# Performance work log

Hardware: AMD Instinct MI355X
Metric: run time of the kernel (lower is better)

Reference implementation:

```python
import jax, jax.numpy as jnp
import numpy as np

D_MODEL = 2048
N_HEADS = 32
N_KV_HEADS = 8
HEAD_DIM = D_MODEL // N_HEADS  # 64
THETA = 10000.0
BATCH = 2
SEQ = 2048


def _rope_tables(seq_len, head_dim, theta):
    idx = jnp.arange(0, head_dim, 2, dtype=jnp.float32)
    inv_freq = 1.0 / (theta ** (idx / head_dim))
    pos = jnp.arange(seq_len, dtype=jnp.float32)
    angles = pos[:, None] * inv_freq[None, :]  # (S, head_dim/2)
    return jnp.cos(angles), jnp.sin(angles)


def _apply_rope(x, cos, sin):
    # x: (B, H, S, Dh); cos/sin: (S, Dh/2)
    c = cos[None, None, :, :]
    s = sin[None, None, :, :]
    x_even = x[..., 0::2]
    x_odd = x[..., 1::2]
    out_even = x_even * c - x_odd * s
    out_odd = x_even * s + x_odd * c
    # interleave back: stack on last axis and reshape
    return jnp.stack([out_even, out_odd], axis=-1).reshape(x.shape)


def setup_inputs() -> dict:
    key = jax.random.key(0)
    kx, kq, kk, kv, ko = jax.random.split(key, 5)
    std_sq = (2.0 / (D_MODEL + D_MODEL)) ** 0.5
    std_kv = (2.0 / (D_MODEL + N_KV_HEADS * HEAD_DIM)) ** 0.5
    return {
        "x": jax.random.normal(kx, (BATCH, SEQ, D_MODEL), dtype=jnp.float32),
        "Wq": jax.random.normal(kq, (D_MODEL, D_MODEL), dtype=jnp.float32) * std_sq,
        "Wk": jax.random.normal(kk, (N_KV_HEADS * HEAD_DIM, D_MODEL), dtype=jnp.float32) * std_kv,
        "Wv": jax.random.normal(kv, (N_KV_HEADS * HEAD_DIM, D_MODEL), dtype=jnp.float32) * std_kv,
        "Wo": jax.random.normal(ko, (D_MODEL, D_MODEL), dtype=jnp.float32) * std_sq,
    }


def reference(x, Wq, Wk, Wv, Wo):
    B, S, D = x.shape
    groups = N_HEADS // N_KV_HEADS
    cos, sin = _rope_tables(S, HEAD_DIM, THETA)

    q = (x @ Wq.T).reshape(B, S, N_HEADS, HEAD_DIM).transpose(0, 2, 1, 3)
    k = (x @ Wk.T).reshape(B, S, N_KV_HEADS, HEAD_DIM).transpose(0, 2, 1, 3)
    v = (x @ Wv.T).reshape(B, S, N_KV_HEADS, HEAD_DIM).transpose(0, 2, 1, 3)

    q = _apply_rope(q, cos, sin)
    k = _apply_rope(k, cos, sin)

    # GQA: repeat kv heads (repeat_interleave along head dim)
    k = jnp.repeat(k, groups, axis=1)  # (B, H, S, Dh)
    v = jnp.repeat(v, groups, axis=1)

    scale = 1.0 / jnp.sqrt(jnp.float32(HEAD_DIM))
    scores = jnp.einsum('bhqd,bhkd->bhqk', q, k) * scale
    causal = jnp.tril(jnp.ones((S, S), dtype=bool))
    scores = jnp.where(causal[None, None, :, :], scores, -jnp.inf)
    attn = jax.nn.softmax(scores, axis=-1)
    out = jnp.einsum('bhqk,bhkd->bhqd', attn, v)
    out = out.transpose(0, 2, 1, 3).reshape(B, S, D)
    return out @ Wo.T
```

## Files before the change

### kernel.cpp

```cpp
#include <hip/hip_runtime.h>
#include <math.h>

#define BATCHN 2
#define SEQ 2048
#define DMODEL 2048
#define NH 32
#define NKV 8
#define HDIM 64
#define KVD 512
#define ROWS 4096

typedef __bf16 bf16x8 __attribute__((ext_vector_type(8)));
typedef float f32x4 __attribute__((ext_vector_type(4)));
typedef unsigned short u16x8 __attribute__((ext_vector_type(8)));

#define MFMA(a, b, c) __builtin_amdgcn_mfma_f32_16x16x32_bf16(a, b, c, 0, 0, 0)

__device__ __forceinline__ unsigned short f2bf(float f) {
  union { float f; unsigned u; } v; v.f = f;
  unsigned u = v.u;
  u += 0x7fffu + ((u >> 16) & 1u);
  return (unsigned short)(u >> 16);
}

__device__ __forceinline__ unsigned cvtpk(float a, float b) {
  unsigned r;
  asm("v_cvt_pk_bf16_f32 %0, %1, %2" : "=v"(r) : "v"(a), "v"(b));
  return r;
}
__device__ __forceinline__ void pl32(unsigned& a, unsigned& b) {
  asm("v_permlane32_swap_b32 %0, %1" : "+v"(a), "+v"(b));
}
__device__ __forceinline__ void pl16(unsigned& a, unsigned& b) {
  asm("v_permlane16_swap_b32 %0, %1" : "+v"(a), "+v"(b));
}
__device__ __forceinline__ float exp2v(float x) {
  float r;
  asm("v_exp_f32 %0, %1" : "=v"(r) : "v"(x));
  return r;
}

__device__ __forceinline__ void gload16(const void* g, void* l) {
  __builtin_amdgcn_global_load_lds((const __attribute__((address_space(1))) unsigned int*)g,
                                   (__attribute__((address_space(3))) unsigned int*)l, 16, 0, 0);
}

#define FENCE() asm volatile("" ::: "memory")
#define BARRIER() do { FENCE(); __builtin_amdgcn_s_barrier(); FENCE(); } while (0)
#define VMCNT(n) asm volatile("s_waitcnt vmcnt(" #n ")" ::: "memory")

__global__ __launch_bounds__(256) void conv_all(const float* __restrict__ x,
                                                const float* __restrict__ Wq,
                                                const float* __restrict__ Wk,
                                                const float* __restrict__ Wv,
                                                const float* __restrict__ Wo,
                                                unsigned short* __restrict__ xb,
                                                unsigned short* __restrict__ Wqb,
                                                unsigned short* __restrict__ Wkb,
                                                unsigned short* __restrict__ Wvb,
                                                unsigned short* __restrict__ Wob,
                                                float* __restrict__ ct,
                                                float* __restrict__ st) {
  int i = blockIdx.x * 256 + threadIdx.x;
  const float* in;
  unsigned short* out;
  int off;
  if (i < 2097152)      { in = x;  out = xb;  off = i; }
  else if (i < 3145728) { in = Wq; out = Wqb; off = i - 2097152; }
  else if (i < 3407872) { in = Wk; out = Wkb; off = i - 3145728; }
  else if (i < 3670016) { in = Wv; out = Wvb; off = i - 3407872; }
  else if (i < 4718592) { in = Wo; out = Wob; off = i - 3670016; }
  else {
    int t = i - 4718592;
    int s = t >> 5, f = t & 31;
    float inv = __expf(-(float)f * (9.210340371976184f / 32.0f));
    float ang = (float)s * inv;
    ct[t] = cosf(ang);
    st[t] = sinf(ang);
    return;
  }
  float4 v = ((const float4*)in)[off];
  ushort4 o;
  o.x = f2bf(v.x); o.y = f2bf(v.y); o.z = f2bf(v.z); o.w = f2bf(v.w);
  ((ushort4*)out)[off] = o;
}

__global__ __launch_bounds__(512, 2) void gemm_qkv384(const unsigned short* __restrict__ A,
                                                      const unsigned short* __restrict__ Bq,
                                                      const unsigned short* __restrict__ Bk,
                                                      const unsigned short* __restrict__ Bv,
                                                      unsigned short* __restrict__ Qo,
                                                      unsigned short* __restrict__ Ko,
                                                      unsigned short* __restrict__ Vt,
                                                      const float* __restrict__ ct,
                                                      const float* __restrict__ st) {
  __shared__ __align__(16) unsigned short Als[3][8192];
  __shared__ __align__(16) unsigned short Bls[3][2][8192];
  const int tid = threadIdx.x, lane = tid & 63, wv = tid >> 6;
  const int wm = wv >> 2, wn = wv & 3;
  const int g = lane >> 4, r15 = lane & 15;
  const int c = blockIdx.x & 7, i = blockIdx.x >> 3;
  const int bm = (c >> 1) * 8 + (i & 7);
  const int grp = (c & 1) * 4 + (i >> 3);
  const int row0 = bm << 7;
  const unsigned short* Bpan[3];
  int bnp[3];
#pragma unroll
  for (int bk = 0; bk < 3; ++bk) {
    int p = grp * 3 + bk;
    bnp[bk] = p;
    Bpan[bk] = (p < 16) ? Bq + (size_t)(p << 7) * DMODEL
             : (p < 20) ? Bk + (size_t)((p - 16) << 7) * DMODEL
                        : Bv + (size_t)((p - 20) << 7) * DMODEL;
  }
  const int srow = tid >> 3;
  const int scol = (((tid & 7) ^ ((tid >> 3) & 7)) << 3);
  const unsigned short* gA = A + (size_t)(row0 + srow) * DMODEL + scol;
  const unsigned short* gB0 = Bpan[0] + (size_t)srow * DMODEL + scol;
  const unsigned short* gB1 = Bpan[1] + (size_t)srow * DMODEL + scol;
  const unsigned short* gB2 = Bpan[2] + (size_t)srow * DMODEL + scol;

  f32x4 acc[4][6];
#pragma unroll
  for (int a = 0; a < 4; ++a)
#pragma unroll
    for (int b = 0; b < 6; ++b) acc[a][b] = (f32x4){0.f, 0.f, 0.f, 0.f};

#define STG_A(buf, kt) do { \
    gload16(gA + (size_t)(kt) * 64, &Als[buf][(wv << 9)]); \
    gload16(gA + (size_t)64 * DMODEL + (size_t)(kt) * 64, &Als[buf][4096 + (wv << 9)]); } while (0)
#define STG_B(bank, gp, buf, kt) do { \
    gload16(gp + (size_t)(kt) * 64, &Bls[bank][buf][(wv << 9)]); \
    gload16(gp + (size_t)64 * DMODEL + (size_t)(kt) * 64, &Bls[bank][buf][4096 + (wv << 9)]); } while (0)
#define RA(buf, mf, kk) (*(const bf16x8*)&Als[buf][((wm << 6) + ((mf) << 4) + r15) * 64 + \
                          (((((kk) << 2) + g) ^ (r15 & 7)) << 3)])
#define RB(bank, buf, sub, kk) (*(const bf16x8*)&Bls[bank][buf][((wn << 5) + ((sub) << 4) + r15) * 64 + \
                          (((((kk) << 2) + g) ^ (r15 & 7)) << 3)])

  STG_A(0, 0);
  STG_B(0, gB0, 0, 0); STG_B(1, gB1, 0, 0); STG_B(2, gB2, 0, 0);
  STG_A(1, 1);
  VMCNT(0);
  BARRIER();

  const int NT = DMODEL / 64;
  for (int t = 0; t < NT; ++t) {
    const int ab = t % 3, an2 = (t + 2) % 3;
    const int bb = t & 1, bn2 = bb ^ 1;
    bf16x8 af[4][2];
#pragma unroll
    for (int mf = 0; mf < 4; ++mf) { af[mf][0] = RA(ab, mf, 0); af[mf][1] = RA(ab, mf, 1); }
    bf16x8 b01[2][2][2];
#pragma unroll
    for (int bk = 0; bk < 2; ++bk)
#pragma unroll
      for (int sub = 0; sub < 2; ++sub) {
        b01[bk][sub][0] = RB(bk, bb, sub, 0);
        b01[bk][sub][1] = RB(bk, bb, sub, 1);
      }
    if (t + 1 < NT) {
      STG_B(0, gB0, bn2, t + 1); STG_B(1, gB1, bn2, t + 1); STG_B(2, gB2, bn2, t + 1);
    }
    BARRIER();
    __builtin_amdgcn_s_setprio(1);
#pragma unroll
    for (int mf = 0; mf < 4; ++mf)
#pragma unroll
      for (int bk = 0; bk < 2; ++bk)
#pragma unroll
        for (int sub = 0; sub < 2; ++sub) {
          acc[mf][bk * 2 + sub] = MFMA(af[mf][0], b01[bk][sub][0], acc[mf][bk * 2 + sub]);
          acc[mf][bk * 2 + sub] = MFMA(af[mf][1], b01[bk][sub][1], acc[mf][bk * 2 + sub]);
        }
    __builtin_amdgcn_s_setprio(0);
    BARRIER();
    bf16x8 b2[2][2];
#pragma unroll
    for (int sub = 0; sub < 2; ++sub) { b2[sub][0] = RB(2, bb, sub, 0); b2[sub][1] = RB(2, bb, sub, 1); }
    if (t + 2 < NT) STG_A(an2, t + 2);
    BARRIER();
    __builtin_amdgcn_s_setprio(1);
#pragma unroll
    for (int mf = 0; mf < 4; ++mf)
#pragma unroll
      for (int sub = 0; sub < 2; ++sub) {
        acc[mf][4 + sub] = MFMA(af[mf][0], b2[sub][0], acc[mf][4 + sub]);
        acc[mf][4 + sub] = MFMA(af[mf][1], b2[sub][1], acc[mf][4 + sub]);
      }
    __builtin_amdgcn_s_setprio(0);
    if (t + 2 < NT)      { VMCNT(2); }
    else if (t + 1 < NT) { VMCNT(0); }
    BARRIER();
  }
#undef STG_A
#undef STG_B
#undef RA
#undef RB

  const float QS = 0.18033688011112042f;
#pragma unroll
  for (int bk = 0; bk < 3; ++bk) {
    const int p = bnp[bk];
    if (p < 20) {
      unsigned short* Outb = (p < 16) ? Qo : Ko;
      const int col0 = (p < 16) ? (p << 7) : ((p - 16) << 7);
      const int ldo = (p < 16) ? DMODEL : KVD;
      const int qsc = (p < 16);
#pragma unroll
      for (int mf = 0; mf < 4; ++mf) {
#pragma unroll
        for (int rr = 0; rr < 4; ++rr) {
          const int m = row0 + (wm << 6) + (mf << 4) + (g << 2) + rr;
          const float* ctr = ct + ((m & (SEQ - 1)) << 5);
          const float* str = st + ((m & (SEQ - 1)) << 5);
#pragma unroll
          for (int sub = 0; sub < 2; ++sub) {
            const int n = col0 + (wn << 5) + (sub << 4) + r15;
            float v = acc[mf][bk * 2 + sub][rr];
            float pv = __shfl_xor(v, 1);
            int fi = (n & 63) >> 1;
            float cc = ctr[fi], sn = str[fi];
            v = (lane & 1) ? (pv * sn + v * cc) : (v * cc - pv * sn);
            if (qsc) v *= QS;
            Outb[(size_t)m * ldo + n] = f2bf(v);
          }
        }
      }
    } else {
      const int col0 = (p - 20) << 7;
#pragma unroll
      for (int mf = 0; mf < 4; ++mf) {
        const int m0 = row0 + (wm << 6) + (mf << 4) + (g << 2);
        const int b = m0 >> 11, s0 = m0 & (SEQ - 1);
#pragma unroll
        for (int sub = 0; sub < 2; ++sub) {
          const int nv = col0 + (wn << 5) + (sub << 4) + r15;
          ushort4 o;
          o.x = f2bf(acc[mf][bk * 2 + sub][0]);
          o.y = f2bf(acc[mf][bk * 2 + sub][1]);
          o.z = f2bf(acc[mf][bk * 2 + sub][2]);
          o.w = f2bf(acc[mf][bk * 2 + sub][3]);
          *(ushort4*)(Vt + ((size_t)(b * NKV * HDIM + nv)) * SEQ + s0) = o;
        }
      }
    }
  }
}

__global__ __launch_bounds__(512) void gemm_out128(const unsigned short* __restrict__ A,
                                                   const unsigned short* __restrict__ B,
                                                   float* __restrict__ C) {
  __shared__ __align__(16) unsigned short Als[3][8192];
  __shared__ __align__(16) unsigned short Bls[3][2][8192];
  const int tid = threadIdx.x, lane = tid & 63, wv = tid >> 6;
  const int wm = wv >> 2, wn = wv & 3;
  const int g = lane >> 4, r15 = lane & 15;
  const int wgid = (blockIdx.x & 7) * 32 + (blockIdx.x >> 3);
  const int bm = wgid >> 3, bn = wgid & 7;
  const int row0 = bm << 7, col0 = bn << 8;
  const int srl = tid >> 3;
  const int sgc = ((tid & 7) ^ (srl & 7)) << 3;
  const unsigned short* gA = A + (size_t)(row0 + srl) * DMODEL + sgc;
  const unsigned short* gB = B + (size_t)(col0 + srl) * DMODEL + sgc;

  f32x4 acc[4][4];
#pragma unroll
  for (int i = 0; i < 4; ++i)
#pragma unroll
    for (int jj = 0; jj < 4; ++jj) acc[i][jj] = (f32x4){0.f, 0.f, 0.f, 0.f};

#define STG_A1(buf, kt) do { \
    gload16(gA + (size_t)(kt) * 64, &Als[buf][(wv << 9)]); \
    gload16(gA + (size_t)64 * DMODEL + (size_t)(kt) * 64, &Als[buf][4096 + (wv << 9)]); } while (0)
#define STG_B1(buf, h, kt) do { \
    gload16(gB + (size_t)((h) * 128) * DMODEL + (kt) * 64, &Bls[buf][h][(wv << 9)]); \
    gload16(gB + (size_t)((h) * 128 + 64) * DMODEL + (kt) * 64, &Bls[buf][h][4096 + (wv << 9)]); } while (0)
#define RA1(buf, mf, kk) (*(const bf16x8*)&Als[buf][((wm << 6) + (mf) * 16 + r15) * 64 + \
                           (((((kk) << 2) + g) ^ (r15 & 7)) << 3)])
#define RB1(buf, nf, kk) (*(const bf16x8*)&Bls[buf][wn >> 1][((wn & 1) * 64 + (nf) * 16 + r15) * 64 + \
                           (((((kk) << 2) + g) ^ (r15 & 7)) << 3)])

  STG_B1(0, 0, 0); STG_B1(0, 1, 0); STG_A1(0, 0);
  STG_B1(1, 0, 1); STG_B1(1, 1, 1); STG_A1(1, 1);
  VMCNT(6);
  BARRIER();

  const int NT = DMODEL / 64;
  for (int t = 0; t < NT; ++t) {
    const int cur = t % 3;
    const int stg = (t + 2) % 3;
    bf16x8 a[4][2], b0[2][2];
#pragma unroll
    for (int mf = 0; mf < 4; ++mf) { a[mf][0] = RA1(cur, mf, 0); a[mf][1] = RA1(cur, mf, 1); }
#pragma unroll
    for (int nf = 0; nf < 2; ++nf) { b0[nf][0] = RB1(cur, nf, 0); b0[nf][1] = RB1(cur, nf, 1); }
    if (t + 2 < NT) { STG_B1(stg, 0, t + 2); STG_B1(stg, 1, t + 2); }
    BARRIER();
    __builtin_amdgcn_s_setprio(1);
#pragma unroll
    for (int mf = 0; mf < 4; ++mf)
#pragma unroll
      for (int nf = 0; nf < 2; ++nf) {
        acc[mf][nf] = MFMA(a[mf][0], b0[nf][0], acc[mf][nf]);
        acc[mf][nf] = MFMA(a[mf][1], b0[nf][1], acc[mf][nf]);
      }
    __builtin_amdgcn_s_setprio(0);
    BARRIER();
    bf16x8 b2[2][2];
#pragma unroll
    for (int nf = 0; nf < 2; ++nf) { b2[nf][0] = RB1(cur, 2 + nf, 0); b2[nf][1] = RB1(cur, 2 + nf, 1); }
    if (t + 2 < NT) STG_A1(stg, t + 2);
    BARRIER();
    __builtin_amdgcn_s_setprio(1);
#pragma unroll
    for (int mf = 0; mf < 4; ++mf)
#pragma unroll
      for (int nf = 0; nf < 2; ++nf) {
        acc[mf][2 + nf] = MFMA(a[mf][0], b2[nf][0], acc[mf][2 + nf]);
        acc[mf][2 + nf] = MFMA(a[mf][1], b2[nf][1], acc[mf][2 + nf]);
      }
    __builtin_amdgcn_s_setprio(0);
    if (t + 2 < NT) { VMCNT(6); }
    else if (t + 2 == NT) { VMCNT(0); }
    BARRIER();
  }
#undef STG_A1
#undef STG_B1
#undef RA1
#undef RB1

#pragma unroll
  for (int mf = 0; mf < 4; ++mf)
#pragma unroll
    for (int rr = 0; rr < 4; ++rr) {
      const int m = row0 + (wm << 6) + (mf) * 16 + (g << 2) + rr;
#pragma unroll
      for (int nf = 0; nf < 4; ++nf)
        C[(size_t)m * DMODEL + col0 + (wn << 6) + (nf << 4) + r15] = acc[mf][nf][rr];
    }
}

__global__ __launch_bounds__(512) void attn_fwd(const unsigned short* __restrict__ Q,
                                                const unsigned short* __restrict__ K,
                                                const unsigned short* __restrict__ Vt,
                                                unsigned short* __restrict__ O) {
  __shared__ __align__(16) unsigned short Kls[2][64 * 64];
  __shared__ __align__(16) unsigned short Vls[2][64 * 64];
  const int bid = blockIdx.x;
  const int xcd = bid & 7;
  const int within = bid >> 3;
  const int grp = xcd * 2 + (within >> 5);
  const int w32 = within & 31;
  const int j = w32 & 7;
  const int hsub = w32 >> 3;
  const int b = grp >> 3, kvh = grp & 7;
  const int h = kvh * 4 + hsub;
  const int wave = threadIdx.x >> 6, lane = threadIdx.x & 63;
  const int g = lane >> 4, r15 = lane & 15;
  const int sr = lane >> 3;
  const int sc = (((lane & 7) << 4) ^ (sr << 4)) >> 1;
  const unsigned short* kbase = K + (size_t)b * SEQ * KVD + kvh * HDIM;
  const unsigned short* vbase = Vt + (size_t)((b * NKV + kvh) * HDIM) * SEQ;

  union { u16x8 s; bf16x8 v; } one8;
#pragma unroll
  for (int z = 0; z < 8; ++z) one8.s[z] = 0x3F80;

  auto STAGE = [&](int bi, int kbv) {
    const int r = wave * 8;
    gload16(kbase + (size_t)(kbv + r + sr) * KVD + sc, &Kls[bi][r * 64]);
    gload16(vbase + (size_t)(r + sr) * SEQ + kbv + sc, &Vls[bi][r * 64]);
  };

#pragma unroll 1
  for (int sel = 0; sel < 2; ++sel) {
    const int qt = sel ? (15 - j) : j;
    const int qrow0 = qt * 128 + wave * 16;
    const unsigned short* qp = Q + (size_t)(b * SEQ + qrow0 + r15) * DMODEL + h * HDIM;
    bf16x8 q0 = *(const bf16x8*)(qp + g * 8);
    bf16x8 q1 = *(const bf16x8*)(qp + 32 + g * 8);
    f32x4 oacc[4] = {};
    f32x4 lacc = {};
    const int kend = (qt + 1) * 128;
    __syncthreads();
    STAGE(0, 0);
    int buf = 0;
    for (int kb = 0; kb < kend; kb += 64) {
      __syncthreads();
      if (kb + 64 < kend) STAGE(buf ^ 1, kb + 64);
      const char* Kc = (const char*)&Kls[buf][0];
      const char* Vc = (const char*)&Vls[buf][0];
      f32x4 s[4];
      __builtin_amdgcn_s_setprio(1);
#pragma unroll
      for (int f = 0; f < 4; ++f) {
        const int r = f * 16 + r15;
        const int sw = (r & 7) << 4;
        bf16x8 k0 = *(const bf16x8*)(Kc + r * 128 + ((g * 16) ^ sw));
        bf16x8 k1 = *(const bf16x8*)(Kc + r * 128 + ((64 + g * 16) ^ sw));
        f32x4 z = {};
        s[f] = MFMA(k1, q1, MFMA(k0, q0, z));
      }
      __builtin_amdgcn_s_setprio(0);
      if (kb + 64 > qrow0) {
        const int q = qrow0 + r15;
#pragma unroll
        for (int f = 0; f < 4; ++f)
#pragma unroll
          for (int rr = 0; rr < 4; ++rr)
            if (kb + f * 16 + g * 4 + rr > q) s[f][rr] = -1e30f;
      }
#pragma unroll
      for (int f = 0; f < 4; ++f)
#pragma unroll
        for (int rr = 0; rr < 4; ++rr) s[f][rr] = exp2v(s[f][rr]);
      bf16x8 p1, p2;
      {
        union { bf16x8 v; unsigned u[4]; } P1, P2;
        unsigned a0 = cvtpk(s[0][0], s[0][1]), b0 = cvtpk(s[1][0], s[1][1]);
        pl32(a0, b0); pl16(a0, b0);
        unsigned a1 = cvtpk(s[0][2], s[0][3]), b1 = cvtpk(s[1][2], s[1][3]);
        pl32(a1, b1); pl16(a1, b1);
        P1.u[0] = a0; P1.u[1] = a1; P1.u[2] = b0; P1.u[3] = b1;
        unsigned a2 = cvtpk(s[2][0], s[2][1]), b2 = cvtpk(s[3][0], s[3][1]);
        pl32(a2, b2); pl16(a2, b2);
        unsigned a3 = cvtpk(s[2][2], s[2][3]), b3 = cvtpk(s[3][2], s[3][3]);
        pl32(a3, b3); pl16(a3, b3);
        P2.u[0] = a2; P2.u[1] = a3; P2.u[2] = b2; P2.u[3] = b3;
        p1 = P1.v; p2 = P2.v;
      }
      lacc = MFMA(p2, one8.v, MFMA(p1, one8.v, lacc));
      __builtin_amdgcn_s_setprio(1);
#pragma unroll
      for (int dc = 0; dc < 4; ++dc) {
        const int r = dc * 16 + r15;
        const int sw = (r & 7) << 4;
        bf16x8 v0 = *(const bf16x8*)(Vc + r * 128 + ((g * 16) ^ sw));
        bf16x8 v1 = *(const bf16x8*)(Vc + r * 128 + ((64 + g * 16) ^ sw));
        oacc[dc] = MFMA(p2, v1, MFMA(p1, v0, oacc[dc]));
      }
      __builtin_amdgcn_s_setprio(0);
      buf ^= 1;
    }
    float rls[4];
#pragma unroll
    for (int rr = 0; rr < 4; ++rr) rls[rr] = 1.0f / lacc[rr];
    unsigned short* optr = O + (size_t)(b * SEQ + qrow0) * DMODEL + h * HDIM;
#pragma unroll
    for (int dc = 0; dc < 4; ++dc)
#pragma unroll
      for (int rr = 0; rr < 4; ++rr)
        optr[(size_t)(g * 4 + rr) * DMODEL + dc * 16 + r15] = f2bf(oacc[dc][rr] * rls[rr]);
  }
}

extern "C" void kernel_launch(void* const* d_in, const int* in_sizes, int n_in,
                              void* d_out, int out_size, void* d_ws, size_t ws_size,
                              hipStream_t stream) {
  const float* x  = (const float*)d_in[0];
  const float* Wq = (const float*)d_in[1];
  const float* Wk = (const float*)d_in[2];
  const float* Wv = (const float*)d_in[3];
  const float* Wo = (const float*)d_in[4];

  char* ws = (char*)d_ws;
  unsigned short* xb  = (unsigned short*)(ws);
  unsigned short* Wqb = (unsigned short*)(ws + (16u << 20));
  unsigned short* Wkb = (unsigned short*)(ws + (24u << 20));
  unsigned short* Wvb = (unsigned short*)(ws + (26u << 20));
  unsigned short* Wob = (unsigned short*)(ws + (28u << 20));
  unsigned short* Qb  = (unsigned short*)(ws + (36u << 20));
  unsigned short* Kb  = (unsigned short*)(ws + (52u << 20));
  unsigned short* Vtb = (unsigned short*)(ws + (60u << 20));
  unsigned short* AO  = (unsigned short*)(ws + (64u << 20));
  float* ct = (float*)(ws + (80u << 20));
  float* st = (float*)(ws + (81u << 20));

  conv_all<<<18688, 256, 0, stream>>>(x, Wq, Wk, Wv, Wo, xb, Wqb, Wkb, Wvb, Wob, ct, st);

  gemm_qkv384<<<256, 512, 0, stream>>>(xb, Wqb, Wkb, Wvb, Qb, Kb, Vtb, ct, st);

  attn_fwd<<<512, 512, 0, stream>>>(Qb, Kb, Vtb, AO);

  gemm_out128<<<256, 512, 0, stream>>>(AO, Wob, (float*)d_out);
}
```

Before: 161.9 us.

## Merge GEMM half-iterations and double attention KV staging block to 128 keys

Result: no change. 159.0 us (-1.8%).

```diff
diff --git a/kernel.cpp b/kernel.cpp
--- a/kernel.cpp
+++ b/kernel.cpp
@@ -289,12 +289,14 @@
   for (int t = 0; t < NT; ++t) {
     const int cur = t % 3;
     const int stg = (t + 2) % 3;
-    bf16x8 a[4][2], b0[2][2];
+    bf16x8 a[4][2], b0[2][2], b2[2][2];
 #pragma unroll
     for (int mf = 0; mf < 4; ++mf) { a[mf][0] = RA1(cur, mf, 0); a[mf][1] = RA1(cur, mf, 1); }
 #pragma unroll
     for (int nf = 0; nf < 2; ++nf) { b0[nf][0] = RB1(cur, nf, 0); b0[nf][1] = RB1(cur, nf, 1); }
-    if (t + 2 < NT) { STG_B1(stg, 0, t + 2); STG_B1(stg, 1, t + 2); }
+#pragma unroll
+    for (int nf = 0; nf < 2; ++nf) { b2[nf][0] = RB1(cur, 2 + nf, 0); b2[nf][1] = RB1(cur, 2 + nf, 1); }
+    if (t + 2 < NT) { STG_B1(stg, 0, t + 2); STG_B1(stg, 1, t + 2); STG_A1(stg, t + 2); }
     BARRIER();
     __builtin_amdgcn_s_setprio(1);
 #pragma unroll
@@ -303,19 +305,6 @@
       for (int nf = 0; nf < 2; ++nf) {
         acc[mf][nf] = MFMA(a[mf][0], b0[nf][0], acc[mf][nf]);
         acc[mf][nf] = MFMA(a[mf][1], b0[nf][1], acc[mf][nf]);
-      }
-    __builtin_amdgcn_s_setprio(0);
-    BARRIER();
-    bf16x8 b2[2][2];
-#pragma unroll
-    for (int nf = 0; nf < 2; ++nf) { b2[nf][0] = RB1(cur, 2 + nf, 0); b2[nf][1] = RB1(cur, 2 + nf, 1); }
-    if (t + 2 < NT) STG_A1(stg, t + 2);
-    BARRIER();
-    __builtin_amdgcn_s_setprio(1);
-#pragma unroll
-    for (int mf = 0; mf < 4; ++mf)
-#pragma unroll
-      for (int nf = 0; nf < 2; ++nf) {
         acc[mf][2 + nf] = MFMA(a[mf][0], b2[nf][0], acc[mf][2 + nf]);
         acc[mf][2 + nf] = MFMA(a[mf][1], b2[nf][1], acc[mf][2 + nf]);
       }
@@ -344,8 +333,8 @@
                                                 const unsigned short* __restrict__ K,
                                                 const unsigned short* __restrict__ Vt,
                                                 unsigned short* __restrict__ O) {
-  __shared__ __align__(16) unsigned short Kls[2][64 * 64];
-  __shared__ __align__(16) unsigned short Vls[2][64 * 64];
+  __shared__ __align__(16) unsigned short Kls[2][2][64 * 64];
+  __shared__ __align__(16) unsigned short Vls[2][2][64 * 64];
   const int bid = blockIdx.x;
   const int xcd = bid & 7;
   const int within = bid >> 3;
@@ -368,8 +357,11 @@
 
   auto STAGE = [&](int bi, int kbv) {
     const int r = wave * 8;
-    gload16(kbase + (size_t)(kbv + r + sr) * KVD + sc, &Kls[bi][r * 64]);
-    gload16(vbase + (size_t)(r + sr) * SEQ + kbv + sc, &Vls[bi][r * 64]);
+#pragma unroll
+    for (int hh = 0; hh < 2; ++hh) {
+      gload16(kbase + (size_t)(kbv + hh * 64 + r + sr) * KVD + sc, &Kls[bi][hh][r * 64]);
+      gload16(vbase + (size_t)(r + sr) * SEQ + kbv + hh * 64 + sc, &Vls[bi][hh][r * 64]);
+    }
   };
 
 #pragma unroll 1
@@ -385,61 +377,65 @@
     __syncthreads();
     STAGE(0, 0);
     int buf = 0;
-    for (int kb = 0; kb < kend; kb += 64) {
+    for (int kb = 0; kb < kend; kb += 128) {
       __syncthreads();
-      if (kb + 64 < kend) STAGE(buf ^ 1, kb + 64);
-      const char* Kc = (const char*)&Kls[buf][0];
-      const char* Vc = (const char*)&Vls[buf][0];
-      f32x4 s[4];
-      __builtin_amdgcn_s_setprio(1);
-#pragma unroll
-      for (int f = 0; f < 4; ++f) {
-        const int r = f * 16 + r15;
-        const int sw = (r & 7) << 4;
-        bf16x8 k0 = *(const bf16x8*)(Kc + r * 128 + ((g * 16) ^ sw));
-        bf16x8 k1 = *(const bf16x8*)(Kc + r * 128 + ((64 + g * 16) ^ sw));
-        f32x4 z = {};
-        s[f] = MFMA(k1, q1, MFMA(k0, q0, z));
-      }
-      __builtin_amdgcn_s_setprio(0);
-      if (kb + 64 > qrow0) {
-        const int q = qrow0 + r15;
+      if (kb + 128 < kend) STAGE(buf ^ 1, kb + 128);
+#pragma unroll
+      for (int hh = 0; hh < 2; ++hh) {
+        const char* Kc = (const char*)&Kls[buf][hh][0];
+        const char* Vc = (const char*)&Vls[buf][hh][0];
+        const int cb = kb + hh * 64;
+        f32x4 s[4];
+        __builtin_amdgcn_s_setprio(1);
+#pragma unroll
+        for (int f = 0; f < 4; ++f) {
+          const int r = f * 16 + r15;
+          const int sw = (r & 7) << 4;
+          bf16x8 k0 = *(const bf16x8*)(Kc + r * 128 + ((g * 16) ^ sw));
+          bf16x8 k1 = *(const bf16x8*)(Kc + r * 128 + ((64 + g * 16) ^ sw));
+          f32x4 z = {};
+          s[f] = MFMA(k1, q1, MFMA(k0, q0, z));
+        }
+        __builtin_amdgcn_s_setprio(0);
+        if (cb + 64 > qrow0) {
+          const int q = qrow0 + r15;
+#pragma unroll
+          for (int f = 0; f < 4; ++f)
+#pragma unroll
+            for (int rr = 0; rr < 4; ++rr)
+              if (cb + f * 16 + g * 4 + rr > q) s[f][rr] = -1e30f;
+        }
 #pragma unroll
         for (int f = 0; f < 4; ++f)
 #pragma unroll
-          for (int rr = 0; rr < 4; ++rr)
-            if (kb + f * 16 + g * 4 + rr > q) s[f][rr] = -1e30f;
-      }
-#pragma unroll
-      for (int f = 0; f < 4; ++f)
-#pragma unroll
-        for (int rr = 0; rr < 4; ++rr) s[f][rr] = exp2v(s[f][rr]);
-      bf16x8 p1, p2;
-      {
-        union { bf16x8 v; unsigned u[4]; } P1, P2;
-        unsigned a0 = cvtpk(s[0][0], s[0][1]), b0 = cvtpk(s[1][0], s[1][1]);
-        pl32(a0, b0); pl16(a0, b0);
-        unsigned a1 = cvtpk(s[0][2], s[0][3]), b1 = cvtpk(s[1][2], s[1][3]);
-        pl32(a1, b1); pl16(a1, b1);
-        P1.u[0] = a0; P1.u[1] = a1; P1.u[2] = b0; P1.u[3] = b1;
-        unsigned a2 = cvtpk(s[2][0], s[2][1]), b2 = cvtpk(s[3][0], s[3][1]);
-        pl32(a2, b2); pl16(a2, b2);
-        unsigned a3 = cvtpk(s[2][2], s[2][3]), b3 = cvtpk(s[3][2], s[3][3]);
-        pl32(a3, b3); pl16(a3, b3);
-        P2.u[0] = a2; P2.u[1] = a3; P2.u[2] = b2; P2.u[3] = b3;
-        p1 = P1.v; p2 = P2.v;
-      }
-      lacc = MFMA(p2, one8.v, MFMA(p1, one8.v, lacc));
-      __builtin_amdgcn_s_setprio(1);
-#pragma unroll
-      for (int dc = 0; dc < 4; ++dc) {
-        const int r = dc * 16 + r15;
-        const int sw = (r & 7) << 4;
-        bf16x8 v0 = *(const bf16x8*)(Vc + r * 128 + ((g * 16) ^ sw));
-        bf16x8 v1 = *(const bf16x8*)(Vc + r * 128 + ((64 + g * 16) ^ sw));
-        oacc[dc] = MFMA(p2, v1, MFMA(p1, v0, oacc[dc]));
-      }
-      __builtin_amdgcn_s_setprio(0);
+          for (int rr = 0; rr < 4; ++rr) s[f][rr] = exp2v(s[f][rr]);
+        bf16x8 p1, p2;
+        {
+          union { bf16x8 v; unsigned u[4]; } P1, P2;
+          unsigned a0 = cvtpk(s[0][0], s[0][1]), b0 = cvtpk(s[1][0], s[1][1]);
+          pl32(a0, b0); pl16(a0, b0);
+          unsigned a1 = cvtpk(s[0][2], s[0][3]), b1 = cvtpk(s[1][2], s[1][3]);
+          pl32(a1, b1); pl16(a1, b1);
+          P1.u[0] = a0; P1.u[1] = a1; P1.u[2] = b0; P1.u[3] = b1;
+          unsigned a2 = cvtpk(s[2][0], s[2][1]), b2 = cvtpk(s[3][0], s[3][1]);
+          pl32(a2, b2); pl16(a2, b2);
+          unsigned a3 = cvtpk(s[2][2], s[2][3]), b3 = cvtpk(s[3][2], s[3][3]);
+          pl32(a3, b3); pl16(a3, b3);
+          P2.u[0] = a2; P2.u[1] = a3; P2.u[2] = b2; P2.u[3] = b3;
+          p1 = P1.v; p2 = P2.v;
+        }
+        lacc = MFMA(p2, one8.v, MFMA(p1, one8.v, lacc));
+        __builtin_amdgcn_s_setprio(1);
+#pragma unroll
+        for (int dc = 0; dc < 4; ++dc) {
+          const int r = dc * 16 + r15;
+          const int sw = (r & 7) << 4;
+          bf16x8 v0 = *(const bf16x8*)(Vc + r * 128 + ((g * 16) ^ sw));
+          bf16x8 v1 = *(const bf16x8*)(Vc + r * 128 + ((64 + g * 16) ^ sw));
+          oacc[dc] = MFMA(p2, v1, MFMA(p1, v0, oacc[dc]));
+        }
+        __builtin_amdgcn_s_setprio(0);
+      }
       buf ^= 1;
     }
     float rls[4];
```
